# Optimization experiments

Measured on AMD Instinct MI355X. Metric: run time of the kernel, lower is better.

## Reference

```python
import jax, jax.numpy as jnp
import numpy as np

C = 512
NUM_HEADS = 8
GROUPS = 32
EPS = 1e-5


def setup_inputs() -> dict:
    key = jax.random.key(0)
    ks = jax.random.split(key, 7)
    B, H, W = 8, 32, 32
    x = jax.random.normal(ks[0], (B, C, H, W), dtype=jnp.float32)
    gn_w = jnp.ones((C,), dtype=jnp.float32)
    gn_b = jnp.zeros((C,), dtype=jnp.float32)
    # 1x1 convs as dense matrices [out, in]
    qkv_w = jax.random.normal(ks[1], (3 * C, C), dtype=jnp.float32) * (1.0 / np.sqrt(C))
    qkv_b = jnp.zeros((3 * C,), dtype=jnp.float32)
    proj_w = jax.random.normal(ks[2], (C, C), dtype=jnp.float32) * (1.0 / np.sqrt(C))
    proj_b = jnp.zeros((C,), dtype=jnp.float32)
    return {"x": x, "gn_w": gn_w, "gn_b": gn_b, "qkv_w": qkv_w,
            "qkv_b": qkv_b, "proj_w": proj_w, "proj_b": proj_b}


def reference(x, gn_w, gn_b, qkv_w, qkv_b, proj_w, proj_b):
    B, Cc, H, W = x.shape
    nh = NUM_HEADS
    d = Cc // nh
    N = H * W

    # GroupNorm(32, C) with affine
    xg = x.reshape(B, GROUPS, Cc // GROUPS, H, W)
    mean = jnp.mean(xg, axis=(2, 3, 4), keepdims=True)
    var = jnp.var(xg, axis=(2, 3, 4), keepdims=True)
    hn = ((xg - mean) * jax.lax.rsqrt(var + EPS)).reshape(B, Cc, H, W)
    hn = hn * gn_w[None, :, None, None] + gn_b[None, :, None, None]

    # 1x1 conv QKV projection: [B, 3C, H, W]
    qkv = jnp.einsum('oc,bchw->bohw', qkv_w, hn) + qkv_b[None, :, None, None]
    q, k, v = jnp.split(qkv, 3, axis=1)

    def to_heads(t):  # [B, C, H, W] -> [B, nh, N, d]
        return t.reshape(B, nh, d, N).transpose(0, 1, 3, 2)

    q, k, v = to_heads(q), to_heads(k), to_heads(v)
    scale = d ** (-0.5)
    attn = jax.nn.softmax(jnp.einsum('bhnd,bhmd->bhnm', q, k) * scale, axis=-1)
    o = jnp.einsum('bhnm,bhmd->bhnd', attn, v)          # [B, nh, N, d]
    o = o.transpose(0, 1, 3, 2).reshape(B, Cc, H, W)

    # 1x1 conv output projection + residual
    o = jnp.einsum('oc,bchw->bohw', proj_w, o) + proj_b[None, :, None, None]
    return x + o
```

## Files before the change

### kernel.cpp

```cpp
#include <hip/hip_runtime.h>

typedef __bf16 bf16x8 __attribute__((ext_vector_type(8)));
typedef float f32x4 __attribute__((ext_vector_type(4)));

#define MFMA(a, b, c) __builtin_amdgcn_mfma_f32_16x16x32_bf16(a, b, c, 0, 0, 0)

#define CS 0.18033688011112042f

__device__ __forceinline__ ushort f2bf(float f) {
    __bf16 h = (__bf16)f;
    return *(ushort*)&h;
}
__device__ __forceinline__ float bf2f(ushort u) {
    unsigned int x = ((unsigned int)u) << 16;
    return __uint_as_float(x);
}

__device__ __forceinline__ void stage_tile64(ushort* lds, const ushort* gbase,
                                             int row_stride, int nchunks,
                                             int wave, int lane) {
    int r8 = lane >> 3;
    int cswz = ((lane & 7) ^ r8) << 4;
#pragma unroll
    for (int c = wave; c < nchunks; c += 4) {
        const char* g = (const char*)(gbase + (size_t)(c * 8 + r8) * row_stride) + cswz;
        __builtin_amdgcn_global_load_lds(
            (const __attribute__((address_space(1))) unsigned int*)g,
            (__attribute__((address_space(3))) unsigned int*)((char*)lds + c * 1024),
            16, 0, 0);
    }
}

__device__ __forceinline__ bf16x8 lds_read_row(const ushort* lds, int row, int cb) {
    return *(const bf16x8*)((const char*)lds + row * 128 + (cb ^ ((row & 7) << 4)));
}

__device__ __forceinline__ void stage_tile32(ushort* lds, const ushort* gbase,
                                             int row_stride, int nchunks,
                                             int wave, int lane) {
    int r16 = lane >> 2;
    int csw = (((lane & 3) ^ ((lane >> 3) & 3)) << 3);
#pragma unroll
    for (int c = wave; c < nchunks; c += 4) {
        const ushort* g = gbase + (size_t)(c * 16 + r16) * row_stride + csw;
        __builtin_amdgcn_global_load_lds(
            (const __attribute__((address_space(1))) unsigned int*)g,
            (__attribute__((address_space(3))) unsigned int*)((char*)lds + c * 1024),
            16, 0, 0);
    }
}

__device__ __forceinline__ bf16x8 lds_read_row32(const ushort* lds, int row, int cb) {
    return *(const bf16x8*)((const char*)lds + row * 64 + (cb ^ (((row >> 1) & 3) << 4)));
}

__global__ __launch_bounds__(256) void gn_cvt_kernel(const float* __restrict__ x,
                                                     const float* __restrict__ gnw,
                                                     const float* __restrict__ gnb,
                                                     ushort* __restrict__ hnT,
                                                     const float* __restrict__ w1,
                                                     const float* __restrict__ w2,
                                                     ushort* __restrict__ o1,
                                                     ushort* __restrict__ o2) {
    __shared__ ushort xcache[16 * 1028];
    __shared__ float red[8];
    __shared__ float sw[16], sb[16];

    if (blockIdx.x >= 256) {
        int t = (blockIdx.x - 256) * 256 + threadIdx.x;
        const int n1q = (1536 * 512) / 4;
        float4 v;
        ushort* dst;
        int idx;
        if (t < n1q) {
            v = ((const float4*)w1)[t]; dst = o1; idx = t;
        } else {
            idx = t - n1q;
            v = ((const float4*)w2)[idx]; dst = o2;
        }
        ushort4 p;
        p.x = f2bf(v.x); p.y = f2bf(v.y); p.z = f2bf(v.z); p.w = f2bf(v.w);
        ((ushort4*)dst)[idx] = p;
        return;
    }

    int b = blockIdx.x >> 5, g = blockIdx.x & 31;
    const float* xp = x + (size_t)(b * 512 + g * 16) * 1024;
    int t = threadIdx.x;

    float s = 0.f, ss = 0.f;
    const float4* xp4 = (const float4*)xp;
    for (int i = t; i < 4096; i += 256) {
        float4 v = xp4[i];
        s += (v.x + v.y) + (v.z + v.w);
        ss += (v.x * v.x + v.y * v.y) + (v.z * v.z + v.w * v.w);
        int f = i * 4;
        int cc = f >> 10, nl = f & 1023;
        ushort4 c;
        c.x = f2bf(v.x); c.y = f2bf(v.y); c.z = f2bf(v.z); c.w = f2bf(v.w);
        *(ushort4*)&xcache[cc * 1028 + nl] = c;
    }
#pragma unroll
    for (int off = 32; off >= 1; off >>= 1) {
        s += __shfl_xor(s, off);
        ss += __shfl_xor(ss, off);
    }
    int wave = t >> 6;
    if ((t & 63) == 0) { red[wave] = s; red[wave + 4] = ss; }
    if (t < 16) { sw[t] = gnw[g * 16 + t]; sb[t] = gnb[g * 16 + t]; }
    __syncthreads();
    float S = red[0] + red[1] + red[2] + red[3];
    float SS = red[4] + red[5] + red[6] + red[7];
    float mean = S * (1.0f / 16384.0f);
    float var = SS * (1.0f / 16384.0f) - mean * mean;
    float rstd = rsqrtf(var + 1e-5f);

    int cc0 = (t & 3) * 4;
    int nb = t >> 2;
    float w0 = sw[cc0] * rstd, w1_ = sw[cc0 + 1] * rstd,
          w2_ = sw[cc0 + 2] * rstd, w3 = sw[cc0 + 3] * rstd;
    float b0 = sb[cc0] - mean * w0, b1 = sb[cc0 + 1] - mean * w1_,
          b2 = sb[cc0 + 2] - mean * w2_, b3 = sb[cc0 + 3] - mean * w3;
#pragma unroll
    for (int k = 0; k < 16; ++k) {
        int nl = nb + 64 * k;
        ushort4 p;
        p.x = f2bf(bf2f(xcache[(cc0 + 0) * 1028 + nl]) * w0 + b0);
        p.y = f2bf(bf2f(xcache[(cc0 + 1) * 1028 + nl]) * w1_ + b1);
        p.z = f2bf(bf2f(xcache[(cc0 + 2) * 1028 + nl]) * w2_ + b2);
        p.w = f2bf(bf2f(xcache[(cc0 + 3) * 1028 + nl]) * w3 + b3);
        *(ushort4*)(hnT + ((size_t)b * 1024 + nl) * 512 + g * 16 + cc0) = p;
    }
}

__global__ __launch_bounds__(256, 3) void gemm_qkv(const ushort* __restrict__ Wb,
                                                   const ushort* __restrict__ hnT,
                                                   const float* __restrict__ qkvb,
                                                   ushort* __restrict__ qT,
                                                   ushort* __restrict__ kT,
                                                   ushort* __restrict__ vb) {
    int lane = threadIdx.x & 63, wave = threadIdx.x >> 6;
    int l15 = lane & 15, lg = lane >> 4;
    int bi = blockIdx.x;
    int b = bi & 7;
    int slot = bi >> 3;
    int m0 = (slot % 12) * 128;
    int n0 = (slot / 12) * 128;
    int mw = (wave >> 1) * 64, nw = (wave & 1) * 64;
    const ushort* Ag = Wb + (size_t)m0 * 512;
    const ushort* Bg = hnT + (size_t)b * 524288 + (size_t)n0 * 512;

    __shared__ ushort abuf[3][4096];
    __shared__ ushort bbuf[3][4096];

    f32x4 acc[4][4] = {};
#pragma unroll
    for (int p = 0; p < 2; ++p) {
        stage_tile32(abuf[p], Ag + p * 32, 512, 8, wave, lane);
        stage_tile32(bbuf[p], Bg + p * 32, 512, 8, wave, lane);
    }
    asm volatile("s_waitcnt vmcnt(4)" ::: "memory");
    __builtin_amdgcn_s_barrier();

    int cur = 0;
#pragma unroll 1
    for (int t = 0; t < 16; ++t) {
        if (t < 14) {
            int nxt = cur + 2; if (nxt >= 3) nxt -= 3;
            stage_tile32(abuf[nxt], Ag + (t + 2) * 32, 512, 8, wave, lane);
            stage_tile32(bbuf[nxt], Bg + (t + 2) * 32, 512, 8, wave, lane);
        }
        const ushort* A = abuf[cur];
        const ushort* B = bbuf[cur];
        bf16x8 af[4], bfr[4];
#pragma unroll
        for (int i = 0; i < 4; i++)
            af[i] = lds_read_row32(A, mw + i * 16 + l15, lg * 16);
#pragma unroll
        for (int j = 0; j < 4; j++)
            bfr[j] = lds_read_row32(B, nw + j * 16 + l15, lg * 16);
        __builtin_amdgcn_s_setprio(1);
#pragma unroll
        for (int i = 0; i < 4; i++)
#pragma unroll
            for (int j = 0; j < 4; j++)
                acc[i][j] = MFMA(af[i], bfr[j], acc[i][j]);
        __builtin_amdgcn_s_setprio(0);
        if (t < 15) {
            if (t < 14) asm volatile("s_waitcnt vmcnt(4)" ::: "memory");
            else        asm volatile("s_waitcnt vmcnt(0)" ::: "memory");
            __builtin_amdgcn_s_barrier();
        }
        cur = cur + 1; if (cur == 3) cur = 0;
    }

#pragma unroll
    for (int i = 0; i < 4; i++) {
        int ob = m0 + mw + i * 16 + lg * 4;
        float bias[4];
#pragma unroll
        for (int r = 0; r < 4; r++) bias[r] = qkvb[ob + r];
        int part = ob >> 9;
        int oo = ob & 511;
#pragma unroll
        for (int j = 0; j < 4; j++) {
            int n = n0 + nw + j * 16 + l15;
            if (part == 2) {
                int L = n & 63;
                int cf = L >> 4;
                int s = ((cf >> 1) << 5) | (((L >> 2) & 3) << 3) | ((cf & 1) << 2) | (L & 3);
                int np = (n & ~63) | s;
#pragma unroll
                for (int r = 0; r < 4; r++)
                    vb[(size_t)(b * 512 + oo + r) * 1024 + np] = f2bf(acc[i][j][r] + bias[r]);
            } else {
                ushort* dst = part ? kT : qT;
                float sc = part ? 1.0f : CS;
                int h = oo >> 6, dd = oo & 63;
                ushort4 p;
                p.x = f2bf((acc[i][j][0] + bias[0]) * sc);
                p.y = f2bf((acc[i][j][1] + bias[1]) * sc);
                p.z = f2bf((acc[i][j][2] + bias[2]) * sc);
                p.w = f2bf((acc[i][j][3] + bias[3]) * sc);
                *(ushort4*)(dst + ((size_t)((b * 8 + h) * 1024 + n)) * 64 + dd) = p;
            }
        }
    }
}

__global__ __launch_bounds__(256) void attn_kernel(const ushort* __restrict__ qT,
                                                   const ushort* __restrict__ kT,
                                                   const ushort* __restrict__ vb,
                                                   ushort* __restrict__ aoT) {
    int bi = blockIdx.x;
    int bh = ((bi >> 6) << 3) | (bi & 7);
    int q0 = ((bi >> 3) & 7) * 128;
    int b = bh >> 3, h = bh & 7;
    int lane = threadIdx.x & 63, wave = threadIdx.x >> 6;
    int l15 = lane & 15, lg = lane >> 4;
    const ushort* qp = qT + (size_t)bh * 65536;
    const ushort* kp = kT + (size_t)bh * 65536;
    const ushort* vp = vb + (size_t)bh * 65536;

    __shared__ ushort kbuf[3][4096];
    __shared__ ushort vbuf[3][4096];

    bf16x8 vone;
#pragma unroll
    for (int e = 0; e < 8; e++) vone[e] = (__bf16)1.0f;

    bf16x8 qf[2][2];
#pragma unroll
    for (int i = 0; i < 2; i++)
#pragma unroll
        for (int kh = 0; kh < 2; kh++)
            qf[i][kh] = *(const bf16x8*)(qp + (size_t)(q0 + wave * 32 + i * 16 + l15) * 64 + kh * 32 + lg * 8);

    f32x4 oacc[2][4] = {};
    f32x4 lacc[2] = {};

    stage_tile64(kbuf[0], kp, 64, 8, wave, lane);
    stage_tile64(vbuf[0], vp, 1024, 8, wave, lane);
    stage_tile64(kbuf[1], kp + 4096, 64, 8, wave, lane);
    stage_tile64(vbuf[1], vp + 64, 1024, 8, wave, lane);
    asm volatile("s_waitcnt vmcnt(4)" ::: "memory");
    __builtin_amdgcn_s_barrier();

    int cur = 0;
#pragma unroll 1
    for (int t = 0; t < 16; ++t) {
        if (t < 14) {
            int nxt = cur + 2; if (nxt >= 3) nxt -= 3;
            stage_tile64(kbuf[nxt], kp + (size_t)(t + 2) * 4096, 64, 8, wave, lane);
            stage_tile64(vbuf[nxt], vp + (t + 2) * 64, 1024, 8, wave, lane);
        }
        const ushort* kb = kbuf[cur];
        const ushort* vc = vbuf[cur];

        f32x4 sacc[2][4] = {};
        __builtin_amdgcn_s_setprio(1);
#pragma unroll
        for (int kh = 0; kh < 2; kh++)
#pragma unroll
            for (int cf = 0; cf < 4; cf++) {
                bf16x8 kf = lds_read_row(kb, cf * 16 + l15, kh * 64 + lg * 16);
                sacc[0][cf] = MFMA(kf, qf[0][kh], sacc[0][cf]);
                sacc[1][cf] = MFMA(kf, qf[1][kh], sacc[1][cf]);
            }
        __builtin_amdgcn_s_setprio(0);

        bf16x8 vf[2][4];
#pragma unroll
        for (int ks = 0; ks < 2; ks++)
#pragma unroll
            for (int cf = 0; cf < 4; cf++)
                vf[ks][cf] = lds_read_row(vc, cf * 16 + l15, ks * 64 + lg * 16);

        bf16x8 pa[2][2];
#pragma unroll
        for (int i = 0; i < 2; i++)
#pragma unroll
            for (int ks = 0; ks < 2; ks++) {
                bf16x8 tr;
#pragma unroll
                for (int jhi = 0; jhi < 2; jhi++)
#pragma unroll
                    for (int r = 0; r < 4; r++)
                        tr[jhi * 4 + r] = (__bf16)exp2f(sacc[i][ks * 2 + jhi][r]);
                pa[i][ks] = tr;
            }

        __builtin_amdgcn_s_setprio(1);
#pragma unroll
        for (int i = 0; i < 2; i++)
#pragma unroll
            for (int ks = 0; ks < 2; ks++) {
                lacc[i] = MFMA(pa[i][ks], vone, lacc[i]);
#pragma unroll
                for (int cf = 0; cf < 4; cf++)
                    oacc[i][cf] = MFMA(pa[i][ks], vf[ks][cf], oacc[i][cf]);
            }
        __builtin_amdgcn_s_setprio(0);

        if (t < 15) {
            if (t < 14) asm volatile("s_waitcnt vmcnt(4)" ::: "memory");
            else        asm volatile("s_waitcnt vmcnt(0)" ::: "memory");
            __builtin_amdgcn_s_barrier();
        }
        cur = cur + 1; if (cur == 3) cur = 0;
    }

#pragma unroll
    for (int i = 0; i < 2; i++)
#pragma unroll
        for (int r = 0; r < 4; r++) {
            float inv = 1.0f / lacc[i][r];
            int n = q0 + wave * 32 + i * 16 + lg * 4 + r;
            size_t obase = ((size_t)b * 1024 + n) * 512 + h * 64;
#pragma unroll
            for (int cf = 0; cf < 4; cf++)
                aoT[obase + cf * 16 + l15] = f2bf(oacc[i][cf][r] * inv);
        }
}

__global__ __launch_bounds__(256) void gemm_proj(const ushort* __restrict__ Wb,
                                                 const ushort* __restrict__ aoT,
                                                 const float* __restrict__ projb,
                                                 const float* __restrict__ x,
                                                 float* __restrict__ out) {
    int lane = threadIdx.x & 63, wave = threadIdx.x >> 6;
    int l15 = lane & 15, lg = lane >> 4;
    int bi = blockIdx.x;
    int b = bi & 7;
    int slot = bi >> 3;
    int m0 = (slot & 3) * 128;
    int n0 = (slot >> 2) * 64;
    int mw = (wave >> 1) * 64, nw = (wave & 1) * 32;
    const ushort* Ag = Wb + (size_t)m0 * 512;
    const ushort* Bg = aoT + (size_t)b * 524288 + (size_t)n0 * 512;

    __shared__ ushort abuf[4][4096];
    __shared__ ushort bbuf[4][2048];

    f32x4 acc[4][2] = {};
#pragma unroll
    for (int p = 0; p < 3; ++p) {
        stage_tile32(abuf[p], Ag + p * 32, 512, 8, wave, lane);
        stage_tile32(bbuf[p], Bg + p * 32, 512, 4, wave, lane);
    }
    asm volatile("s_waitcnt vmcnt(6)" ::: "memory");
    __builtin_amdgcn_s_barrier();

#pragma unroll 1
    for (int t = 0; t < 16; ++t) {
        if (t < 13) {
            int nxt = (t + 3) & 3;
            stage_tile32(abuf[nxt], Ag + (t + 3) * 32, 512, 8, wave, lane);
            stage_tile32(bbuf[nxt], Bg + (t + 3) * 32, 512, 4, wave, lane);
        }
        const ushort* A = abuf[t & 3];
        const ushort* B = bbuf[t & 3];
        bf16x8 af[4], bfr[2];
#pragma unroll
        for (int i = 0; i < 4; i++)
            af[i] = lds_read_row32(A, mw + i * 16 + l15, lg * 16);
#pragma unroll
        for (int j = 0; j < 2; j++)
            bfr[j] = lds_read_row32(B, nw + j * 16 + l15, lg * 16);
        __builtin_amdgcn_s_setprio(1);
#pragma unroll
        for (int i = 0; i < 4; i++)
#pragma unroll
            for (int j = 0; j < 2; j++)
                acc[i][j] = MFMA(af[i], bfr[j], acc[i][j]);
        __builtin_amdgcn_s_setprio(0);
        if (t < 15) {
            if (t < 13)      asm volatile("s_waitcnt vmcnt(6)" ::: "memory");
            else if (t == 13) asm volatile("s_waitcnt vmcnt(3)" ::: "memory");
            else              asm volatile("s_waitcnt vmcnt(0)" ::: "memory");
            __builtin_amdgcn_s_barrier();
        }
    }

#pragma unroll
    for (int i = 0; i < 4; i++) {
        int ob = m0 + mw + i * 16 + lg * 4;
        float bias[4];
#pragma unroll
        for (int r = 0; r < 4; r++) bias[r] = projb[ob + r];
#pragma unroll
        for (int j = 0; j < 2; j++) {
            int n = n0 + nw + j * 16 + l15;
#pragma unroll
            for (int r = 0; r < 4; r++) {
                size_t idx = (size_t)(b * 512 + ob + r) * 1024 + n;
                out[idx] = x[idx] + bias[r] + acc[i][j][r];
            }
        }
    }
}

extern "C" void kernel_launch(void* const* d_in, const int* in_sizes, int n_in,
                              void* d_out, int out_size, void* d_ws, size_t ws_size,
                              hipStream_t stream) {
    const float* x     = (const float*)d_in[0];
    const float* gnw   = (const float*)d_in[1];
    const float* gnb   = (const float*)d_in[2];
    const float* qkvw  = (const float*)d_in[3];
    const float* qkvb  = (const float*)d_in[4];
    const float* projw = (const float*)d_in[5];
    const float* projb = (const float*)d_in[6];
    float* out = (float*)d_out;

    char* ws = (char*)d_ws;
    ushort* hnT    = (ushort*)(ws);
    ushort* qT     = (ushort*)(ws + (size_t)(8u << 20));
    ushort* kT     = (ushort*)(ws + (size_t)(16u << 20));
    ushort* vbuf   = (ushort*)(ws + (size_t)(24u << 20));
    ushort* qkvwb  = (ushort*)(ws + (size_t)(32u << 20));
    ushort* projwb = (ushort*)(ws + (size_t)(32u << 20) + 1572864);

    gn_cvt_kernel<<<dim3(1280), dim3(256), 0, stream>>>(x, gnw, gnb, hnT,
                                                        qkvw, projw, qkvwb, projwb);
    gemm_qkv<<<dim3(768), dim3(256), 0, stream>>>(qkvwb, hnT, qkvb, qT, kT, vbuf);
    attn_kernel<<<dim3(512), dim3(256), 0, stream>>>(qT, kT, vbuf, hnT );
    gemm_proj<<<dim3(512), dim3(256), 0, stream>>>(projwb, hnT, projb, x, out);
}
```

Before: 80.20 us.

## Use two waves per attention block, each handling 64 query rows

The attention block drops from four waves to two, and each wave now processes 64 query rows instead of 32. K and V fragments are read from LDS once per tile and reused across two 32-row halves, which halves LDS read traffic per query. Each wave issues twice as many staging loads, so the wait counts are adjusted to match. The trade-off is higher register pressure from the larger accumulators and fewer waves per block to hide latency, since there are still 512 blocks with the same LDS use.

```diff
diff --git a/kernel.cpp b/kernel.cpp
--- a/kernel.cpp
+++ b/kernel.cpp
@@ -23,6 +23,21 @@
     int cswz = ((lane & 7) ^ r8) << 4;
 #pragma unroll
     for (int c = wave; c < nchunks; c += 4) {
+        const char* g = (const char*)(gbase + (size_t)(c * 8 + r8) * row_stride) + cswz;
+        __builtin_amdgcn_global_load_lds(
+            (const __attribute__((address_space(1))) unsigned int*)g,
+            (__attribute__((address_space(3))) unsigned int*)((char*)lds + c * 1024),
+            16, 0, 0);
+    }
+}
+
+__device__ __forceinline__ void stage_tile64w2(ushort* lds, const ushort* gbase,
+                                               int row_stride, int nchunks,
+                                               int wave, int lane) {
+    int r8 = lane >> 3;
+    int cswz = ((lane & 7) ^ r8) << 4;
+#pragma unroll
+    for (int c = wave; c < nchunks; c += 2) {
         const char* g = (const char*)(gbase + (size_t)(c * 8 + r8) * row_stride) + cswz;
         __builtin_amdgcn_global_load_lds(
             (const __attribute__((address_space(1))) unsigned int*)g,
@@ -228,7 +243,7 @@
     }
 }
 
-__global__ __launch_bounds__(256) void attn_kernel(const ushort* __restrict__ qT,
+__global__ __launch_bounds__(128) void attn_kernel(const ushort* __restrict__ qT,
                                                    const ushort* __restrict__ kT,
                                                    const ushort* __restrict__ vb,
                                                    ushort* __restrict__ aoT) {
@@ -249,21 +264,22 @@
 #pragma unroll
     for (int e = 0; e < 8; e++) vone[e] = (__bf16)1.0f;
 
-    bf16x8 qf[2][2];
-#pragma unroll
-    for (int i = 0; i < 2; i++)
+    int qbase = q0 + wave * 64;
+    bf16x8 qf[4][2];
+#pragma unroll
+    for (int i = 0; i < 4; i++)
 #pragma unroll
         for (int kh = 0; kh < 2; kh++)
-            qf[i][kh] = *(const bf16x8*)(qp + (size_t)(q0 + wave * 32 + i * 16 + l15) * 64 + kh * 32 + lg * 8);
-
-    f32x4 oacc[2][4] = {};
-    f32x4 lacc[2] = {};
-
-    stage_tile64(kbuf[0], kp, 64, 8, wave, lane);
-    stage_tile64(vbuf[0], vp, 1024, 8, wave, lane);
-    stage_tile64(kbuf[1], kp + 4096, 64, 8, wave, lane);
-    stage_tile64(vbuf[1], vp + 64, 1024, 8, wave, lane);
-    asm volatile("s_waitcnt vmcnt(4)" ::: "memory");
+            qf[i][kh] = *(const bf16x8*)(qp + (size_t)(qbase + i * 16 + l15) * 64 + kh * 32 + lg * 8);
+
+    f32x4 oacc[4][4] = {};
+    f32x4 lacc[4] = {};
+
+    stage_tile64w2(kbuf[0], kp, 64, 8, wave, lane);
+    stage_tile64w2(vbuf[0], vp, 1024, 8, wave, lane);
+    stage_tile64w2(kbuf[1], kp + 4096, 64, 8, wave, lane);
+    stage_tile64w2(vbuf[1], vp + 64, 1024, 8, wave, lane);
+    asm volatile("s_waitcnt vmcnt(8)" ::: "memory");
     __builtin_amdgcn_s_barrier();
 
     int cur = 0;
@@ -271,59 +287,66 @@
     for (int t = 0; t < 16; ++t) {
         if (t < 14) {
             int nxt = cur + 2; if (nxt >= 3) nxt -= 3;
-            stage_tile64(kbuf[nxt], kp + (size_t)(t + 2) * 4096, 64, 8, wave, lane);
-            stage_tile64(vbuf[nxt], vp + (t + 2) * 64, 1024, 8, wave, lane);
+            stage_tile64w2(kbuf[nxt], kp + (size_t)(t + 2) * 4096, 64, 8, wave, lane);
+            stage_tile64w2(vbuf[nxt], vp + (t + 2) * 64, 1024, 8, wave, lane);
         }
         const ushort* kb = kbuf[cur];
         const ushort* vc = vbuf[cur];
 
-        f32x4 sacc[2][4] = {};
-        __builtin_amdgcn_s_setprio(1);
+        bf16x8 kf[2][4], vf[2][4];
 #pragma unroll
         for (int kh = 0; kh < 2; kh++)
 #pragma unroll
-            for (int cf = 0; cf < 4; cf++) {
-                bf16x8 kf = lds_read_row(kb, cf * 16 + l15, kh * 64 + lg * 16);
-                sacc[0][cf] = MFMA(kf, qf[0][kh], sacc[0][cf]);
-                sacc[1][cf] = MFMA(kf, qf[1][kh], sacc[1][cf]);
-            }
-        __builtin_amdgcn_s_setprio(0);
-
-        bf16x8 vf[2][4];
+            for (int cf = 0; cf < 4; cf++)
+                kf[kh][cf] = lds_read_row(kb, cf * 16 + l15, kh * 64 + lg * 16);
 #pragma unroll
         for (int ks = 0; ks < 2; ks++)
 #pragma unroll
             for (int cf = 0; cf < 4; cf++)
                 vf[ks][cf] = lds_read_row(vc, cf * 16 + l15, ks * 64 + lg * 16);
 
-        bf16x8 pa[2][2];
-#pragma unroll
-        for (int i = 0; i < 2; i++)
-#pragma unroll
-            for (int ks = 0; ks < 2; ks++) {
-                bf16x8 tr;
-#pragma unroll
-                for (int jhi = 0; jhi < 2; jhi++)
-#pragma unroll
-                    for (int r = 0; r < 4; r++)
-                        tr[jhi * 4 + r] = (__bf16)exp2f(sacc[i][ks * 2 + jhi][r]);
-                pa[i][ks] = tr;
-            }
-
-        __builtin_amdgcn_s_setprio(1);
-#pragma unroll
-        for (int i = 0; i < 2; i++)
-#pragma unroll
-            for (int ks = 0; ks < 2; ks++) {
-                lacc[i] = MFMA(pa[i][ks], vone, lacc[i]);
-#pragma unroll
-                for (int cf = 0; cf < 4; cf++)
-                    oacc[i][cf] = MFMA(pa[i][ks], vf[ks][cf], oacc[i][cf]);
-            }
-        __builtin_amdgcn_s_setprio(0);
+#pragma unroll
+        for (int ih = 0; ih < 2; ih++) {
+            f32x4 sacc[2][4] = {};
+            __builtin_amdgcn_s_setprio(1);
+#pragma unroll
+            for (int kh = 0; kh < 2; kh++)
+#pragma unroll
+                for (int cf = 0; cf < 4; cf++) {
+                    sacc[0][cf] = MFMA(kf[kh][cf], qf[2 * ih + 0][kh], sacc[0][cf]);
+                    sacc[1][cf] = MFMA(kf[kh][cf], qf[2 * ih + 1][kh], sacc[1][cf]);
+                }
+            __builtin_amdgcn_s_setprio(0);
+
+            bf16x8 pa[2][2];
+#pragma unroll
+            for (int ii = 0; ii < 2; ii++)
+#pragma unroll
+                for (int ks = 0; ks < 2; ks++) {
+                    bf16x8 tr;
+#pragma unroll
+                    for (int jhi = 0; jhi < 2; jhi++)
+#pragma unroll
+                        for (int r = 0; r < 4; r++)
+                            tr[jhi * 4 + r] = (__bf16)exp2f(sacc[ii][ks * 2 + jhi][r]);
+                    pa[ii][ks] = tr;
+                }
+
+            __builtin_amdgcn_s_setprio(1);
+#pragma unroll
+            for (int ii = 0; ii < 2; ii++)
+#pragma unroll
+                for (int ks = 0; ks < 2; ks++) {
+                    lacc[2 * ih + ii] = MFMA(pa[ii][ks], vone, lacc[2 * ih + ii]);
+#pragma unroll
+                    for (int cf = 0; cf < 4; cf++)
+                        oacc[2 * ih + ii][cf] = MFMA(pa[ii][ks], vf[ks][cf], oacc[2 * ih + ii][cf]);
+                }
+            __builtin_amdgcn_s_setprio(0);
+        }
 
         if (t < 15) {
-            if (t < 14) asm volatile("s_waitcnt vmcnt(4)" ::: "memory");
+            if (t < 14) asm volatile("s_waitcnt vmcnt(8)" ::: "memory");
             else        asm volatile("s_waitcnt vmcnt(0)" ::: "memory");
             __builtin_amdgcn_s_barrier();
         }
@@ -331,11 +354,11 @@
     }
 
 #pragma unroll
-    for (int i = 0; i < 2; i++)
+    for (int i = 0; i < 4; i++)
 #pragma unroll
         for (int r = 0; r < 4; r++) {
             float inv = 1.0f / lacc[i][r];
-            int n = q0 + wave * 32 + i * 16 + lg * 4 + r;
+            int n = qbase + i * 16 + lg * 4 + r;
             size_t obase = ((size_t)b * 1024 + n) * 512 + h * 64;
 #pragma unroll
             for (int cf = 0; cf < 4; cf++)
@@ -443,6 +466,6 @@
     gn_cvt_kernel<<<dim3(1280), dim3(256), 0, stream>>>(x, gnw, gnb, hnT,
                                                         qkvw, projw, qkvwb, projwb);
     gemm_qkv<<<dim3(768), dim3(256), 0, stream>>>(qkvwb, hnT, qkvb, qT, kT, vbuf);
-    attn_kernel<<<dim3(512), dim3(256), 0, stream>>>(qT, kT, vbuf, hnT );
+    attn_kernel<<<dim3(512), dim3(128), 0, stream>>>(qT, kT, vbuf, hnT );
     gemm_proj<<<dim3(512), dim3(256), 0, stream>>>(projwb, hnT, projb, x, out);
 }
```

New measurement: 87.37 us. 8.9% more time.
